# Performance work log

Measured on AMD Instinct MI355X. Metric: run time of the kernel, lower is better.

The kernel has to match this reference:

```python
import jax, jax.numpy as jnp
import numpy as np
from jax import lax

C = 128      # channels
H = 128
W = 128
B = 2
WS = 4       # window size
HEADS = 4
HID = int(C * 2.66)  # 340
EPS = 1e-6


def conv1x1(x, w):
    # x: [b,c,h,w], w: [out,in]
    return jnp.einsum('oc,bchw->bohw', w, x)


def dwconv3(x, w):
    # depthwise 3x3, w: [c,1,3,3]
    return lax.conv_general_dilated(
        x, w, window_strides=(1, 1), padding='SAME',
        feature_group_count=x.shape[1],
        dimension_numbers=('NCHW', 'OIHW', 'NCHW'))


def layernorm(x, w, b):
    # channel-wise LN over dim 1 (per pixel), w/b: [C]
    m = x.mean(axis=1, keepdims=True)
    v = ((x - m) ** 2).mean(axis=1, keepdims=True)
    xn = (x - m) / jnp.sqrt(v + EPS)
    return xn * w[None, :, None, None] + b[None, :, None, None]


def l2norm(x):
    n = jnp.sqrt(jnp.sum(x * x, axis=-1, keepdims=True))
    return x / jnp.maximum(n, 1e-12)


def rsa(x, qkv_w, dw_w, proj_w, temp):
    b, c, h, w = x.shape
    ws = WS
    x_ = jnp.roll(x, (-ws // 2, -ws // 2), axis=(2, 3))  # shifts > 0
    qkv = dwconv3(conv1x1(x_, qkv_w), dw_w)
    q, k, v = jnp.split(qkv, 3, axis=1)

    def win(t):  # b c (h dh) (w dw) -> b (h w) (dh dw) c
        return t.reshape(b, c, h // ws, ws, w // ws, ws) \
                .transpose(0, 2, 4, 3, 5, 1) \
                .reshape(b, (h // ws) * (w // ws), ws * ws, c)

    q, k, v = win(q), win(k), win(v)
    q = l2norm(q)
    k = l2norm(k)
    # attn = q^T @ k  -> [b, nw, c, c]
    attn = jax.nn.relu(jnp.einsum('bnpc,bnpd->bncd', q, k) * temp[0, 0, 0])
    out = jnp.einsum('bnpc,bncd->bnpd', v, attn)  # v @ attn
    out = out.reshape(b, h // ws, w // ws, ws, ws, c) \
             .transpose(0, 5, 1, 3, 2, 4).reshape(b, c, h, w)
    out = jnp.roll(out, (ws // 2, ws // 2), axis=(2, 3))
    return conv1x1(out, proj_w)


def gsa(x, qkv_w, dw_w, proj_w, temp):
    b, c, h, w = x.shape
    hd = HEADS
    ch = c // hd
    qkv = dwconv3(conv1x1(x, qkv_w), dw_w)
    q, k, v = jnp.split(qkv, 3, axis=1)

    def hs(t):  # b (head c) h w -> b head c (h w)
        return t.reshape(b, hd, ch, h * w)

    q, k, v = hs(q), hs(k), hs(v)
    q = l2norm(q)
    k = l2norm(k)
    attn = jax.nn.relu(jnp.einsum('bhcn,bhdn->bhcd', q, k) * temp[0, 0, 0])
    out = jnp.einsum('bhcd,bhdn->bhcn', attn, v).reshape(b, c, h, w)
    return conv1x1(out, proj_w)


def ffn(x, w_in, w_dw, w_out):
    h = dwconv3(conv1x1(x, w_in), w_dw)
    h = jax.nn.gelu(h, approximate=False)
    return conv1x1(h, w_out)


def setup_inputs() -> dict:
    key = jax.random.key(0)
    ks = jax.random.split(key, 16)
    s = 0.05
    d = {
        'x': jax.random.normal(ks[0], (B, C, H, W), jnp.float32),
        # spatial (RSA) branch
        'w_s0': jnp.ones((C,), jnp.float32), 'b_s0': jnp.zeros((C,), jnp.float32),
        'w_s2': jnp.ones((C,), jnp.float32), 'b_s2': jnp.zeros((C,), jnp.float32),
        'rsa_qkv': jax.random.normal(ks[1], (3 * C, C), jnp.float32) * s,
        'rsa_dw': jax.random.normal(ks[2], (3 * C, 1, 3, 3), jnp.float32) * s,
        'rsa_proj': jax.random.normal(ks[3], (C, C), jnp.float32) * s,
        'rsa_temp': jnp.ones((1, 1, 1), jnp.float32),
        'ffs_in': jax.random.normal(ks[4], (HID, C), jnp.float32) * s,
        'ffs_dw': jax.random.normal(ks[5], (HID, 1, 3, 3), jnp.float32) * s,
        'ffs_out': jax.random.normal(ks[6], (C, HID), jnp.float32) * s,
        # channel (GSA) branch
        'w_c0': jnp.ones((C,), jnp.float32), 'b_c0': jnp.zeros((C,), jnp.float32),
        'w_c2': jnp.ones((C,), jnp.float32), 'b_c2': jnp.zeros((C,), jnp.float32),
        'gsa_qkv': jax.random.normal(ks[7], (3 * C, C), jnp.float32) * s,
        'gsa_dw': jax.random.normal(ks[8], (3 * C, 1, 3, 3), jnp.float32) * s,
        'gsa_proj': jax.random.normal(ks[9], (C, C), jnp.float32) * s,
        'gsa_temp': jnp.ones((1, 1, 1), jnp.float32),
        'ffc_in': jax.random.normal(ks[10], (HID, C), jnp.float32) * s,
        'ffc_dw': jax.random.normal(ks[11], (HID, 1, 3, 3), jnp.float32) * s,
        'ffc_out': jax.random.normal(ks[12], (C, HID), jnp.float32) * s,
    }
    return d


def reference(x, w_s0, b_s0, w_s2, b_s2, rsa_qkv, rsa_dw, rsa_proj, rsa_temp,
              ffs_in, ffs_dw, ffs_out,
              w_c0, b_c0, w_c2, b_c2, gsa_qkv, gsa_dw, gsa_proj, gsa_temp,
              ffc_in, ffc_dw, ffc_out):
    # shared_depth = 1: only the i==0 branches execute
    # spatial block (RSA)
    x_ = rsa(layernorm(x, w_s0, b_s0), rsa_qkv, rsa_dw, rsa_proj, rsa_temp)
    x = ffn(layernorm(x_ + x, w_s2, b_s2), ffs_in, ffs_dw, ffs_out) + x_
    # channel block (GSA)
    x_ = gsa(layernorm(x, w_c0, b_c0), gsa_qkv, gsa_dw, gsa_proj, gsa_temp)
    x = ffn(layernorm(x_ + x, w_c2, b_c2), ffc_in, ffc_dw, ffc_out) + x_
    return x
```

## Files before the change

### kernel.cpp

```cpp
#include <hip/hip_runtime.h>
#include <hip/hip_bf16.h>
#include <math.h>

typedef __hip_bfloat16 bf16;
typedef __attribute__((ext_vector_type(8))) short short8;
typedef __attribute__((ext_vector_type(4))) short short4v;
typedef __attribute__((ext_vector_type(4))) float float4v;

static constexpr int cB  = 2;
static constexpr int cC  = 128;
static constexpr int cH  = 128;
static constexpr int cW  = 128;
static constexpr int cP  = cH * cW;
static constexpr int cC3 = 384;
static constexpr int cHID = 340;
static constexpr int cNW = 1024;
static constexpr float cEPS = 1e-6f;

__device__ __forceinline__ float bfu2f(unsigned short u){
  union { unsigned int i; float f; } c; c.i = ((unsigned int)u) << 16; return c.f;
}
__device__ __forceinline__ unsigned short f2b(float f){
  union { float f; unsigned int u; } c; c.f = f;
  unsigned int r = c.u + 0x7FFFu + ((c.u >> 16) & 1u);
  return (unsigned short)(r >> 16);
}

__global__ void k_wcvt(const float* __restrict__ qkv_s, const float* __restrict__ qkv_c,
                       const float* __restrict__ fin_s, const float* __restrict__ fin_c,
                       const float* __restrict__ prj_s, const float* __restrict__ prj_c,
                       const float* __restrict__ fo_s,  const float* __restrict__ fo_c,
                       unsigned short* __restrict__ WB, float* __restrict__ S){
  int i = blockIdx.x * 256 + threadIdx.x;
  if (i >= 319488){
    int j = i - 319488;
    if (j < 8704) S[j] = 0.f;
    return;
  }
  float v;
  if (i < 98304){
    v = (i < 49152) ? qkv_s[i] : qkv_c[i - 49152];
  } else if (i < 196608){
    int j = (i < 147456) ? (i - 98304) : (i - 147456);
    int row = j >> 7, col = j & 127;
    const float* src = (i < 147456) ? fin_s : fin_c;
    v = (row < cHID) ? src[row * 128 + col] : 0.f;
  } else if (i < 229376){
    v = (i < 212992) ? prj_s[i - 196608] : prj_c[i - 212992];
  } else {
    int j = (i < 274432) ? (i - 229376) : (i - 274432);
    int row = j / 352, col = j - row * 352;
    const float* src = (i < 274432) ? fo_s : fo_c;
    v = (col < cHID) ? src[row * cHID + col] : 0.f;
  }
  WB[i] = f2b(v);
}

__global__ void __launch_bounds__(256) k_gemmLN(const unsigned short* __restrict__ Wb,
                                                const float* __restrict__ Xf,
                                                const float* __restrict__ gamma,
                                                const float* __restrict__ beta,
                                                unsigned short* __restrict__ Out){
  __shared__ short Xls[64 * 136];
  __shared__ short Wls[128 * 40];
  __shared__ float gls[128], bls[128];
  __shared__ float psum[64], pssq[64];
  int bid = blockIdx.x;
  int s  = (bid & 7) * 192 + (bid >> 3);
  int mt = s % 3;
  int r3 = s / 3;
  int pt = r3 & 255;
  int b  = r3 >> 8;
  int p0 = pt * 64;
  int m0 = mt * 128;
  int t  = threadIdx.x;
  int px = t & 63, cq = t >> 6;
  if (t < 64){ psum[t] = 0.f; pssq[t] = 0.f; }
  if (t < 128){ gls[t] = gamma[t]; bls[t] = beta[t]; }
  int rh = p0 >> 7, w0 = p0 & 127;
  int hs = (rh + 2) & (cH - 1);
  int sp = hs * cW + ((w0 + 2 + px) & (cW - 1));
  const float* xb = Xf + (size_t)b * cC * cP + sp;
  float xr[32];
  float s1 = 0.f, s2 = 0.f;
  #pragma unroll
  for (int j = 0; j < 32; j++){
    float v = xb[(size_t)(cq * 32 + j) * cP];
    xr[j] = v; s1 += v; s2 += v * v;
  }
  __syncthreads();
  atomicAdd(&psum[px], s1);
  atomicAdd(&pssq[px], s2);
  __syncthreads();
  float mean = psum[px] * (1.f / cC);
  float var  = pssq[px] * (1.f / cC) - mean * mean;
  float rstd = rsqrtf(var + cEPS);
  #pragma unroll
  for (int k = 0; k < 4; k++){
    short8 tv;
    #pragma unroll
    for (int e = 0; e < 8; e++){
      int c = cq * 32 + k * 8 + e;
      tv[e] = (short)f2b((xr[k * 8 + e] - mean) * rstd * gls[c] + bls[c]);
    }
    *(short8*)&Xls[px * 136 + cq * 32 + k * 8] = tv;
  }
  int lanelo = t & 15;
  int quad   = (t >> 4) & 3;
  int wv = t >> 6;
  int w1 = wv & 1;
  int w2 = wv >> 1;
  int srw = t >> 1;
  int kow = (t & 1) * 16;
  float4v acc[2][4];
  #pragma unroll
  for (int i = 0; i < 2; i++)
    #pragma unroll
    for (int j = 0; j < 4; j++)
      acc[i][j] = (float4v){0.f, 0.f, 0.f, 0.f};
  const unsigned short* Wp = Wb + (size_t)(m0 + srw) * 128 + kow;
  short8 a0 = *(const short8*)(Wp);
  short8 a1 = *(const short8*)(Wp + 8);
  for (int k0 = 0; k0 < 128; k0 += 32){
    __syncthreads();
    *(short8*)&Wls[srw * 40 + kow]     = a0;
    *(short8*)&Wls[srw * 40 + kow + 8] = a1;
    __syncthreads();
    if (k0 < 96){
      a0 = *(const short8*)(Wp + k0 + 32);
      a1 = *(const short8*)(Wp + k0 + 40);
    }
    short8 af[2], bfr[4];
    #pragma unroll
    for (int i = 0; i < 2; i++)
      af[i] = *(const short8*)&Xls[(w1 * 32 + i * 16 + lanelo) * 136 + k0 + quad * 8];
    #pragma unroll
    for (int j = 0; j < 4; j++)
      bfr[j] = *(const short8*)&Wls[(w2 * 64 + j * 16 + lanelo) * 40 + quad * 8];
    #pragma unroll
    for (int i = 0; i < 2; i++)
      #pragma unroll
      for (int j = 0; j < 4; j++)
        acc[i][j] = __builtin_amdgcn_mfma_f32_16x16x32_bf16(af[i], bfr[j], acc[i][j], 0, 0, 0);
  }
  __syncthreads();
  #pragma unroll
  for (int i = 0; i < 2; i++)
    #pragma unroll
    for (int j = 0; j < 4; j++){
      int pixloc = w1 * 32 + i * 16 + quad * 4;
      int mloc   = w2 * 64 + j * 16 + lanelo;
      #pragma unroll
      for (int r = 0; r < 4; r++)
        Xls[(pixloc + r) * 136 + mloc] = (short)f2b(acc[i][j][r]);
    }
  __syncthreads();
  unsigned short* Ob = Out + (size_t)b * cP * cC3;
  #pragma unroll
  for (int rr = 0; rr < 4; rr++){
    int id = t + rr * 256;
    int row = id >> 4, col8 = (id & 15) * 8;
    *(short8*)(Ob + (size_t)(p0 + row) * cC3 + m0 + col8) = *(const short8*)&Xls[row * 136 + col8];
  }
}

__global__ void __launch_bounds__(256) k_gemm(const unsigned short* __restrict__ Wb,
                                              const unsigned short* __restrict__ Xg,
                                              unsigned short* __restrict__ Out,
                                              int K, int PK, int PM){
  __shared__ short SMEM[8704];
  short* Wls = SMEM;
  short* Xls = SMEM + 5120;
  int bid = blockIdx.x;
  int s  = (bid & 7) * (1536 >> 3) + (bid >> 3);
  int mt = s % 3;
  int r3 = s / 3;
  int pt = r3 & 255;
  int b  = r3 >> 8;
  int p0 = pt * 64;
  int m0 = mt * 128;
  int t  = threadIdx.x;
  int lanelo = t & 15;
  int quad   = (t >> 4) & 3;
  int wv = t >> 6;
  int w1 = wv & 1;
  int w2 = wv >> 1;
  int srw = t >> 1;
  int kow = (t & 1) * 16;
  int srx = t >> 2;
  int kox = (t & 3) * 8;

  float4v acc[2][4];
  #pragma unroll
  for (int i = 0; i < 2; i++)
    #pragma unroll
    for (int j = 0; j < 4; j++)
      acc[i][j] = (float4v){0.f, 0.f, 0.f, 0.f};

  const unsigned short* Xp = Xg + (size_t)b * cP * PK + (size_t)(p0 + srx) * PK + kox;
  const unsigned short* Wp = Wb + (size_t)(m0 + srw) * K + kow;

  short8 xv  = *(const short8*)(Xp);
  short8 wv0 = *(const short8*)(Wp);
  short8 wv1 = *(const short8*)(Wp + 8);
  for (int k0 = 0; k0 < K; k0 += 32){
    __syncthreads();
    *(short8*)&Wls[srw * 40 + kow]     = wv0;
    *(short8*)&Wls[srw * 40 + kow + 8] = wv1;
    *(short8*)&Xls[srx * 40 + kox]     = xv;
    __syncthreads();
    if (k0 + 32 < K){
      xv  = *(const short8*)(Xp + k0 + 32);
      wv0 = *(const short8*)(Wp + k0 + 32);
      wv1 = *(const short8*)(Wp + k0 + 40);
    }
    short8 af[2], bfr[4];
    #pragma unroll
    for (int i = 0; i < 2; i++)
      af[i] = *(const short8*)&Xls[(w1 * 32 + i * 16 + lanelo) * 40 + quad * 8];
    #pragma unroll
    for (int j = 0; j < 4; j++)
      bfr[j] = *(const short8*)&Wls[(w2 * 64 + j * 16 + lanelo) * 40 + quad * 8];
    #pragma unroll
    for (int i = 0; i < 2; i++)
      #pragma unroll
      for (int j = 0; j < 4; j++)
        acc[i][j] = __builtin_amdgcn_mfma_f32_16x16x32_bf16(af[i], bfr[j], acc[i][j], 0, 0, 0);
  }
  __syncthreads();
  #pragma unroll
  for (int i = 0; i < 2; i++)
    #pragma unroll
    for (int j = 0; j < 4; j++){
      int pixloc = w1 * 32 + i * 16 + quad * 4;
      int mloc   = w2 * 64 + j * 16 + lanelo;
      #pragma unroll
      for (int r = 0; r < 4; r++)
        SMEM[(pixloc + r) * 136 + mloc] = (short)f2b(acc[i][j][r]);
    }
  __syncthreads();
  unsigned short* Ob = Out + (size_t)b * cP * PM;
  #pragma unroll
  for (int rr = 0; rr < 4; rr++){
    int id = t + rr * 256;
    int row = id >> 4, col8 = (id & 15) * 8;
    int wcol = m0 + col8;
    if (wcol < PM)
      *(short8*)(Ob + (size_t)(p0 + row) * PM + wcol) = *(const short8*)&SMEM[row * 136 + col8];
  }
}

template<int MODE>
__global__ void __launch_bounds__(256) k_gemm64(const unsigned short* __restrict__ Wb,
                                                const unsigned short* __restrict__ Xg,
                                                const float* __restrict__ R,
                                                const float* __restrict__ Base,
                                                const float* __restrict__ gamma,
                                                const float* __restrict__ beta,
                                                float* __restrict__ Tr,
                                                unsigned short* __restrict__ LNo,
                                                int K, int PK){
  __shared__ short SMEM[8704];
  __shared__ float gls[128], bls[128];
  __shared__ float psum[64], pssq[64];
  short* Wls = SMEM;
  short* Xls = SMEM + 5120;
  int b  = blockIdx.z;
  int p0 = blockIdx.x * 64;
  int t  = threadIdx.x;
  int lanelo = t & 15;
  int quad   = (t >> 4) & 3;
  int wv = t >> 6;
  int w2 = wv >> 1, w1 = wv & 1;
  int srw = t >> 1;
  int kow = (t & 1) * 16;
  int srx = t >> 2;
  int kox = (t & 3) * 8;

  if (MODE != 3){
    if (t < 128){ gls[t] = gamma[t]; bls[t] = beta[t]; }
    if (t < 64){ psum[t] = 0.f; pssq[t] = 0.f; }
  }

  float4v acc[4][2];
  #pragma unroll
  for (int i = 0; i < 4; i++){
    acc[i][0] = (float4v){0.f, 0.f, 0.f, 0.f};
    acc[i][1] = (float4v){0.f, 0.f, 0.f, 0.f};
  }
  const unsigned short* Xp = Xg + (size_t)b * cP * PK + (size_t)(p0 + srx) * PK + kox;
  const unsigned short* Wp = Wb + (size_t)srw * K + kow;

  short8 xv  = *(const short8*)(Xp);
  short8 wv0 = *(const short8*)(Wp);
  short8 wv1 = *(const short8*)(Wp + 8);
  for (int k0 = 0; k0 < K; k0 += 32){
    __syncthreads();
    *(short8*)&Wls[srw * 40 + kow]     = wv0;
    *(short8*)&Wls[srw * 40 + kow + 8] = wv1;
    *(short8*)&Xls[srx * 40 + kox]     = xv;
    __syncthreads();
    if (k0 + 32 < K){
      xv  = *(const short8*)(Xp + k0 + 32);
      wv0 = *(const short8*)(Wp + k0 + 32);
      wv1 = *(const short8*)(Wp + k0 + 40);
    }
    short8 af[4], bfr[2];
    #pragma unroll
    for (int i = 0; i < 4; i++)
      af[i] = *(const short8*)&Wls[(w2 * 64 + i * 16 + lanelo) * 40 + quad * 8];
    #pragma unroll
    for (int j = 0; j < 2; j++)
      bfr[j] = *(const short8*)&Xls[(w1 * 32 + j * 16 + lanelo) * 40 + quad * 8];
    #pragma unroll
    for (int i = 0; i < 4; i++)
      #pragma unroll
      for (int j = 0; j < 2; j++)
        acc[i][j] = __builtin_amdgcn_mfma_f32_16x16x32_bf16(af[i], bfr[j], acc[i][j], 0, 0, 0);
  }
  float lnv[4][2][4];
  #pragma unroll
  for (int i = 0; i < 4; i++)
    #pragma unroll
    for (int j = 0; j < 2; j++){
      int n = p0 + w1 * 32 + j * 16 + lanelo;
      #pragma unroll
      for (int r = 0; r < 4; r++){
        int m = w2 * 64 + i * 16 + quad * 4 + r;
        size_t idx = (size_t)b * cC * cP + (size_t)m * cP + n;
        float v = acc[i][j][r];
        if (MODE >= 2) v += R[idx];
        Tr[idx] = v;
        if (MODE == 1) v += Base[idx];
        lnv[i][j][r] = v;
      }
    }
  if (MODE == 3) return;
  __syncthreads();
  #pragma unroll
  for (int j = 0; j < 2; j++){
    int nl = w1 * 32 + j * 16 + lanelo;
    float s = 0.f, ss = 0.f;
    #pragma unroll
    for (int i = 0; i < 4; i++)
      #pragma unroll
      for (int r = 0; r < 4; r++){
        float v = lnv[i][j][r];
        s += v; ss += v * v;
      }
    atomicAdd(&psum[nl], s);
    atomicAdd(&pssq[nl], ss);
  }
  __syncthreads();
  #pragma unroll
  for (int j = 0; j < 2; j++){
    int nl = w1 * 32 + j * 16 + lanelo;
    float mean = psum[nl] * (1.f / cC);
    float var = pssq[nl] * (1.f / cC) - mean * mean;
    float rstd = rsqrtf(var + cEPS);
    #pragma unroll
    for (int i = 0; i < 4; i++)
      #pragma unroll
      for (int r = 0; r < 4; r++){
        int m = w2 * 64 + i * 16 + quad * 4 + r;
        SMEM[nl * 136 + m] = (short)f2b((lnv[i][j][r] - mean) * rstd * gls[m] + bls[m]);
      }
  }
  __syncthreads();
  unsigned short* Ob = LNo + (size_t)b * cP * cC;
  #pragma unroll
  for (int rr = 0; rr < 4; rr++){
    int id = t + rr * 256;
    int row = id >> 4, col8 = (id & 15) * 8;
    short8 sv = *(const short8*)&SMEM[row * 136 + col8];
    *(short8*)(Ob + (size_t)(p0 + row) * cC + col8) = sv;
  }
}

template<int GELU, int CCn, int PITCH>
__global__ void __launch_bounds__(256) k_dw(const unsigned short* __restrict__ in,
                                            const float* __restrict__ wt,
                                            unsigned short* __restrict__ out){
  __shared__ float wls[16 * 76];
  int t = threadIdx.x;
  int cbase = blockIdx.y * 128;
  for (int i = t; i < 16 * 72; i += 256){
    int cg = i / 72, rem = i - cg * 72;
    int tap = rem >> 3, j = rem & 7;
    int c = cbase + cg * 8 + j;
    wls[cg * 76 + rem] = (c < CCn) ? wt[c * 9 + tap] : 0.f;
  }
  __syncthreads();
  int cgl = t & 15, pixl = t >> 4;
  int c0 = cbase + cgl * 8;
  if (c0 >= PITCH) return;
  int p = blockIdx.x * 16 + pixl;
  int h = p >> 7, w = p & 127;
  int b = blockIdx.z;
  const unsigned short* ib = in + (size_t)b * cP * PITCH;
  float4 wreg[18];
  #pragma unroll
  for (int q = 0; q < 18; q++)
    wreg[q] = *(const float4*)&wls[cgl * 76 + q * 4];
  short8 v[9];
  #pragma unroll
  for (int ky = 0; ky < 3; ky++){
    int hh = h + ky - 1;
    bool okh = (unsigned)hh < (unsigned)cH;
    int hc = okh ? hh : h;
    #pragma unroll
    for (int kx = 0; kx < 3; kx++){
      int ww = w + kx - 1;
      bool okw = (unsigned)ww < (unsigned)cW;
      int wc = okw ? ww : w;
      short8 lv = *(const short8*)(ib + (size_t)(hc * cW + wc) * PITCH + c0);
      if (!(okh && okw)) lv = (short8){0,0,0,0,0,0,0,0};
      v[ky * 3 + kx] = lv;
    }
  }
  float acc[8] = {0,0,0,0,0,0,0,0};
  #pragma unroll
  for (int tap = 0; tap < 9; tap++){
    float4 w0 = wreg[tap * 2];
    float4 w1 = wreg[tap * 2 + 1];
    float wa[8] = {w0.x, w0.y, w0.z, w0.w, w1.x, w1.y, w1.z, w1.w};
    #pragma unroll
    for (int j = 0; j < 8; j++)
      acc[j] += wa[j] * bfu2f((unsigned short)v[tap][j]);
  }
  short8 ov;
  #pragma unroll
  for (int j = 0; j < 8; j++){
    float vv = acc[j];
    if (GELU) vv = 0.5f * vv * (1.f + erff(vv * 0.70710678118654752f));
    ov[j] = (short)f2b(vv);
  }
  *(short8*)(out + (size_t)b * cP * PITCH + (size_t)p * PITCH + c0) = ov;
}

__global__ void __launch_bounds__(256) k_rsadw(const unsigned short* __restrict__ qkv,
                                               const float* __restrict__ wt,
                                               const float* __restrict__ temp,
                                               unsigned short* __restrict__ out){
  constexpr int QT = 0;
  constexpr int KT = 5120;
  constexpr int VO = 10240;
  constexpr int HA = 12416;
  constexpr int AT = 12416;
  __shared__ short lds[26528];
  __shared__ float nq[16], nk[16];
  int blk = blockIdx.x;
  int b  = blk >> 10;
  int nw = blk & 1023;
  int hb = nw >> 5, wb = nw & 31;
  int t = threadIdx.x;
  #pragma unroll
  for (int j = 0; j < 5; j++)
    *(short8*)&lds[t * 40 + j * 8] = (short8){0,0,0,0,0,0,0,0};
  if (t < 16) nq[t] = 0.f;
  else if (t < 32) nk[t - 16] = 0.f;
  __syncthreads();
  const unsigned short* base = qkv + (size_t)b * cP * cC3;
  #pragma unroll
  for (int r = 0; r < 7; r++){
    int i = t + 256 * r;
    if (i < 1728){
      int pix6 = i / 48;
      int cg = i - pix6 * 48;
      int hy = pix6 / 6, wx = pix6 - hy * 6;
      int hh = hb * 4 + hy - 1;
      int ww = wb * 4 + wx - 1;
      short8 v = (short8){0,0,0,0,0,0,0,0};
      if ((unsigned)hh < (unsigned)cH && (unsigned)ww < (unsigned)cW)
        v = *(const short8*)(base + (size_t)(hh * cW + ww) * cC3 + cg * 8);
      *(short8*)&lds[HA + pix6 * 392 + cg * 8] = v;
    }
  }
  __syncthreads();
  {
    int px = t & 15, grp = t >> 4;
    int py = px >> 2, pw = px & 3;
    #pragma unroll
    for (int g = 0; g < 3; g++){
      int c0 = grp * 24 + g * 8;
      const float4* wq = (const float4*)(wt + (size_t)c0 * 9);
      float wa[72];
      #pragma unroll
      for (int q = 0; q < 18; q++){
        float4 v4 = wq[q];
        wa[q * 4 + 0] = v4.x; wa[q * 4 + 1] = v4.y;
        wa[q * 4 + 2] = v4.z; wa[q * 4 + 3] = v4.w;
      }
      float acc8[8] = {0,0,0,0,0,0,0,0};
      #pragma unroll
      for (int ky = 0; ky < 3; ky++)
        #pragma unroll
        for (int kx = 0; kx < 3; kx++){
          short8 iv = *(const short8*)&lds[HA + ((py + ky) * 6 + pw + kx) * 392 + c0];
          int tap = ky * 3 + kx;
          #pragma unroll
          for (int e = 0; e < 8; e++)
            acc8[e] += wa[e * 9 + tap] * bfu2f((unsigned short)iv[e]);
        }
      if (c0 < 256){
        int isQ = c0 < 128;
        int off = isQ ? (QT + c0 * 40) : (KT + (c0 - 128) * 40);
        float s = 0.f;
        #pragma unroll
        for (int e = 0; e < 8; e++){
          unsigned short us = f2b(acc8[e]);
          float f = bfu2f(us);
          s += f * f;
          lds[off + e * 40 + px] = (short)us;
        }
        atomicAdd(isQ ? &nq[px] : &nk[px], s);
      } else {
        short8 sv;
        #pragma unroll
        for (int e = 0; e < 8; e++) sv[e] = (short)f2b(acc8[e]);
        *(short8*)&lds[VO + px * 136 + (c0 - 256)] = sv;
      }
    }
  }
  __syncthreads();
  float T = temp[0];
  #pragma unroll
  for (int r = 0; r < 8; r++){
    int idx = t + 256 * r;
    int c = idx >> 4, p = idx & 15;
    float sc = (1.f / fmaxf(sqrtf(nq[p]), 1e-12f)) * (1.f / fmaxf(sqrtf(nk[p]), 1e-12f));
    int a = QT + c * 40 + p;
    lds[a] = (short)f2b(bfu2f((unsigned short)lds[a]) * sc);
  }
  __syncthreads();
  int lanelo = t & 15;
  int quad = (t >> 4) & 3;
  int wv = t >> 6;
  float4v oacc[2];
  oacc[0] = (float4v){0.f,0.f,0.f,0.f};
  oacc[1] = (float4v){0.f,0.f,0.f,0.f};
  for (int ch = 0; ch < 2; ch++){
    #pragma unroll
    for (int ct = 0; ct < 4; ct++){
      int c0 = ch * 64 + ct * 16;
      short8 af = *(const short8*)&lds[QT + (c0 + lanelo) * 40 + quad * 8];
      #pragma unroll
      for (int dt = 0; dt < 2; dt++){
        int d0 = wv * 32 + dt * 16;
        short8 bf = *(const short8*)&lds[KT + (d0 + lanelo) * 40 + quad * 8];
        float4v acc = __builtin_amdgcn_mfma_f32_16x16x32_bf16(af, bf,
                        (float4v){0.f,0.f,0.f,0.f}, 0, 0, 0);
        short4v sv;
        #pragma unroll
        for (int r2 = 0; r2 < 4; r2++) sv[r2] = (short)f2b(fmaxf(acc[r2] * T, 0.f));
        *(short4v*)&lds[AT + (d0 + lanelo) * 72 + ct * 16 + quad * 4] = sv;
      }
    }
    __syncthreads();
    #pragma unroll
    for (int dt = 0; dt < 2; dt++){
      int d0 = wv * 32 + dt * 16;
      #pragma unroll
      for (int kk = 0; kk < 2; kk++){
        short8 av8 = *(const short8*)&lds[VO + lanelo * 136 + ch * 64 + kk * 32 + quad * 8];
        short8 bv8 = *(const short8*)&lds[AT + (d0 + lanelo) * 72 + kk * 32 + quad * 8];
        oacc[dt] = __builtin_amdgcn_mfma_f32_16x16x32_bf16(av8, bv8, oacc[dt], 0, 0, 0);
      }
    }
    __syncthreads();
  }
  #pragma unroll
  for (int dt = 0; dt < 2; dt++){
    int d = wv * 32 + dt * 16 + lanelo;
    #pragma unroll
    for (int r2 = 0; r2 < 4; r2++){
      int p = quad * 4 + r2;
      lds[p * 136 + d] = (short)f2b(oacc[dt][r2]);
    }
  }
  __syncthreads();
  {
    int px = t >> 4, cg = (t & 15) * 8;
    int h2 = (hb * 4 + (px >> 2) + 2) & (cH - 1);
    int w2 = (wb * 4 + (px & 3) + 2) & (cW - 1);
    short8 sv = *(const short8*)&lds[px * 136 + cg];
    *(short8*)(out + (size_t)b * cP * cC + (size_t)(h2 * cW + w2) * cC + cg) = sv;
  }
}

__global__ void __launch_bounds__(256) k_gram(const unsigned short* __restrict__ qkv,
                                              float* __restrict__ S,
                                              float* __restrict__ Qn,
                                              float* __restrict__ Kn){
  __shared__ float qs[32][132];
  __shared__ float ks[32][132];
  int blk = blockIdx.x;
  int chunk = blk & 127;
  int bh = blk >> 7;
  int b = bh >> 2, hd = bh & 3;
  int n0 = chunk * 128;
  int t = threadIdx.x;
  {
    int row = t >> 1;
    int half = t & 1;
    const unsigned short* pq = qkv + (size_t)b * cP * cC3 + (size_t)(n0 + row) * cC3 + hd * 32 + half * 16;
    const unsigned short* pk = pq + 128;
    short8 q0 = *(const short8*)pq;
    short8 q1 = *(const short8*)(pq + 8);
    short8 k0 = *(const short8*)pk;
    short8 k1 = *(const short8*)(pk + 8);
    #pragma unroll
    for (int e = 0; e < 8; e++){
      qs[half * 16 + e][row]     = bfu2f((unsigned short)q0[e]);
      qs[half * 16 + 8 + e][row] = bfu2f((unsigned short)q1[e]);
      ks[half * 16 + e][row]     = bfu2f((unsigned short)k0[e]);
      ks[half * 16 + 8 + e][row] = bfu2f((unsigned short)k1[e]);
    }
  }
  __syncthreads();
  if (t < 64){
    const float* row = (t < 32) ? qs[t] : ks[t - 32];
    float s = 0.f;
    #pragma unroll
    for (int i = 0; i < 128; i += 4){
      float4 v = *(const float4*)(row + i);
      s += v.x*v.x + v.y*v.y + v.z*v.z + v.w*v.w;
    }
    if (t < 32) atomicAdd(&Qn[bh * 32 + t], s);
    else        atomicAdd(&Kn[bh * 32 + (t - 32)], s);
  }
  int cc = (t >> 4) * 2;
  int dd = t & 15;
  float a00 = 0.f, a01 = 0.f, a10 = 0.f, a11 = 0.f;
  for (int n = 0; n < 128; n += 4){
    float4 q0 = *(const float4*)&qs[cc][n];
    float4 q1 = *(const float4*)&qs[cc + 1][n];
    float4 k0 = *(const float4*)&ks[dd][n];
    float4 k1 = *(const float4*)&ks[dd + 16][n];
    a00 += q0.x*k0.x + q0.y*k0.y + q0.z*k0.z + q0.w*k0.w;
    a01 += q0.x*k1.x + q0.y*k1.y + q0.z*k1.z + q0.w*k1.w;
    a10 += q1.x*k0.x + q1.y*k0.y + q1.z*k0.z + q1.w*k0.w;
    a11 += q1.x*k1.x + q1.y*k1.y + q1.z*k1.z + q1.w*k1.w;
  }
  float* Sb = S + (size_t)bh * 1024;
  atomicAdd(&Sb[cc * 32 + dd], a00);
  atomicAdd(&Sb[cc * 32 + dd + 16], a01);
  atomicAdd(&Sb[(cc + 1) * 32 + dd], a10);
  atomicAdd(&Sb[(cc + 1) * 32 + dd + 16], a11);
}

__global__ void __launch_bounds__(256) k_applyM(const unsigned short* __restrict__ qkv,
                                                const float* __restrict__ S,
                                                const float* __restrict__ Qn,
                                                const float* __restrict__ Kn,
                                                const float* __restrict__ temp,
                                                unsigned short* __restrict__ out){
  __shared__ short atb[128 * 40];
  __shared__ short OT[64 * 136];
  int b = blockIdx.y;
  int nbase = blockIdx.x * 64;
  int t = threadIdx.x;
  float T = temp[0];
  #pragma unroll
  for (int it = 0; it < 16; it++){
    int i = t + it * 256;
    int c = i >> 5, d = i & 31;
    int hd = c >> 5, cl = c & 31;
    int bh = b * 4 + hd;
    float nqv = fmaxf(sqrtf(Qn[bh * 32 + cl]), 1e-12f);
    float nkv = fmaxf(sqrtf(Kn[bh * 32 + d]), 1e-12f);
    float v = fmaxf(S[(size_t)bh * 1024 + cl * 32 + d] / (nqv * nkv) * T, 0.f);
    atb[c * 40 + d] = (short)f2b(v);
  }
  __syncthreads();
  int lanelo = t & 15, quad = (t >> 4) & 3, wv = t >> 6;
  int n0 = nbase + wv * 16;
  const unsigned short* vb = qkv + (size_t)b * cP * cC3 + (size_t)(n0 + lanelo) * cC3 + 256 + quad * 8;
  #pragma unroll
  for (int hd = 0; hd < 4; hd++){
    short8 af = *(const short8*)(vb + hd * 32);
    #pragma unroll
    for (int cth = 0; cth < 2; cth++){
      int c0 = hd * 32 + cth * 16;
      short8 bf = *(const short8*)&atb[(c0 + lanelo) * 40 + quad * 8];
      float4v acc = __builtin_amdgcn_mfma_f32_16x16x32_bf16(af, bf,
                      (float4v){0.f,0.f,0.f,0.f}, 0, 0, 0);
      #pragma unroll
      for (int r = 0; r < 4; r++)
        OT[(wv * 16 + quad * 4 + r) * 136 + c0 + lanelo] = (short)f2b(acc[r]);
    }
  }
  __syncthreads();
  unsigned short* ob = out + (size_t)b * cP * cC;
  #pragma unroll
  for (int rr = 0; rr < 4; rr++){
    int id = t + rr * 256;
    int row = id >> 4, col8 = (id & 15) * 8;
    *(short8*)(ob + (size_t)(nbase + row) * cC + col8) = *(const short8*)&OT[row * 136 + col8];
  }
}

extern "C" void kernel_launch(void* const* d_in, const int* in_sizes, int n_in,
                              void* d_out, int out_size, void* d_ws, size_t ws_size,
                              hipStream_t stream){
  const float* x     = (const float*)d_in[0];
  const float* w_s0  = (const float*)d_in[1];
  const float* b_s0  = (const float*)d_in[2];
  const float* w_s2  = (const float*)d_in[3];
  const float* b_s2  = (const float*)d_in[4];
  const float* rsa_qkv  = (const float*)d_in[5];
  const float* rsa_dw   = (const float*)d_in[6];
  const float* rsa_proj = (const float*)d_in[7];
  const float* rsa_temp = (const float*)d_in[8];
  const float* ffs_in   = (const float*)d_in[9];
  const float* ffs_dw   = (const float*)d_in[10];
  const float* ffs_out  = (const float*)d_in[11];
  const float* w_c0  = (const float*)d_in[12];
  const float* b_c0  = (const float*)d_in[13];
  const float* w_c2  = (const float*)d_in[14];
  const float* b_c2  = (const float*)d_in[15];
  const float* gsa_qkv  = (const float*)d_in[16];
  const float* gsa_dw   = (const float*)d_in[17];
  const float* gsa_proj = (const float*)d_in[18];
  const float* gsa_temp = (const float*)d_in[19];
  const float* ffc_in   = (const float*)d_in[20];
  const float* ffc_dw   = (const float*)d_in[21];
  const float* ffc_out  = (const float*)d_in[22];

  const size_t szC  = (size_t)cB * cC * cP;
  const size_t szC3 = (size_t)cB * cC3 * cP;
  float* XF = (float*)d_ws;
  float* XS = XF + szC;
  unsigned short* LO   = (unsigned short*)(XS + szC);
  unsigned short* Abuf = LO + szC;
  unsigned short* Bbuf = Abuf + szC3;
  float* S  = (float*)(Bbuf + szC3);
  float* Qn = S + 8192;
  float* Kn = Qn + 256;
  float* AT = Kn + 256;
  unsigned short* WB = (unsigned short*)(AT + 1024);
  unsigned short* W_QKV_S = WB;
  unsigned short* W_QKV_C = WB + 49152;
  unsigned short* W_FIN_S = WB + 98304;
  unsigned short* W_FIN_C = WB + 147456;
  unsigned short* W_PRJ_S = WB + 196608;
  unsigned short* W_PRJ_C = WB + 212992;
  unsigned short* W_FO_S  = WB + 229376;
  unsigned short* W_FO_C  = WB + 274432;

  dim3 t256(256);
  dim3 gG1(cP / 64 * 3 * cB);
  dim3 gG64(cP / 64, 1, cB);
  dim3 gDW(cP / 16, 3, cB);

  k_wcvt<<<dim3(1282), t256, 0, stream>>>(rsa_qkv, gsa_qkv, ffs_in, ffc_in,
                                          rsa_proj, gsa_proj, ffs_out, ffc_out, WB, S);

  k_gemmLN<<<gG1, t256, 0, stream>>>(W_QKV_S, x, w_s0, b_s0, Abuf);
  k_rsadw<<<dim3(cB * cNW), t256, 0, stream>>>(Abuf, rsa_dw, rsa_temp, LO);
  k_gemm64<1><<<gG64, t256, 0, stream>>>(W_PRJ_S, LO, nullptr, x, w_s2, b_s2, XS, LO, 128, 128);
  k_gemm<<<gG1, t256, 0, stream>>>(W_FIN_S, LO, Abuf, 128, 128, 352);
  k_dw<1,340,352><<<gDW, t256, 0, stream>>>(Abuf, ffs_dw, Bbuf);
  k_gemm64<2><<<gG64, t256, 0, stream>>>(W_FO_S, Bbuf, XS, nullptr, w_c0, b_c0, XF, LO, 352, 352);

  k_gemm<<<gG1, t256, 0, stream>>>(W_QKV_C, LO, Abuf, 128, 128, 384);
  k_dw<0,384,384><<<gDW, t256, 0, stream>>>(Abuf, gsa_dw, Bbuf);
  k_gram<<<dim3(1024), t256, 0, stream>>>(Bbuf, S, Qn, Kn);
  k_applyM<<<dim3(cP / 64, cB), t256, 0, stream>>>(Bbuf, S, Qn, Kn, gsa_temp, LO);
  k_gemm64<1><<<gG64, t256, 0, stream>>>(W_PRJ_C, LO, nullptr, XF, w_c2, b_c2, XS, LO, 128, 128);
  k_gemm<<<gG1, t256, 0, stream>>>(W_FIN_C, LO, Abuf, 128, 128, 352);
  k_dw<1,340,352><<<gDW, t256, 0, stream>>>(Abuf, ffc_dw, Bbuf);
  k_gemm64<3><<<gG64, t256, 0, stream>>>(W_FO_C, Bbuf, XS, nullptr, nullptr, nullptr,
                                         (float*)d_out, nullptr, 352, 352);
}
```

Before: 332.9 us.

## Fuse depthwise 3x3 convs into consuming GEMM, gram and apply kernels

Removes the standalone depthwise-conv kernels. The 3x3 depthwise conv (plus GELU for the FFN paths) is computed on the fly inside the FFN output GEMM's B-operand staging and inside the GSA gram and apply kernels. This drops the write and re-read of the intermediate Bbuf tensor and three launches per block. In exchange it recomputes the depthwise conv in both the gram and apply kernels for V/Q/K, adds nine gathered loads per K-step in the GEMM, and raises LDS use for the depthwise weights.

```diff
diff --git a/kernel.cpp b/kernel.cpp
--- a/kernel.cpp
+++ b/kernel.cpp
@@ -377,65 +377,164 @@
   }
 }
 
-template<int GELU, int CCn, int PITCH>
-__global__ void __launch_bounds__(256) k_dw(const unsigned short* __restrict__ in,
-                                            const float* __restrict__ wt,
-                                            unsigned short* __restrict__ out){
-  __shared__ float wls[16 * 76];
-  int t = threadIdx.x;
-  int cbase = blockIdx.y * 128;
-  for (int i = t; i < 16 * 72; i += 256){
-    int cg = i / 72, rem = i - cg * 72;
-    int tap = rem >> 3, j = rem & 7;
-    int c = cbase + cg * 8 + j;
-    wls[cg * 76 + rem] = (c < CCn) ? wt[c * 9 + tap] : 0.f;
-  }
-  __syncthreads();
-  int cgl = t & 15, pixl = t >> 4;
-  int c0 = cbase + cgl * 8;
-  if (c0 >= PITCH) return;
-  int p = blockIdx.x * 16 + pixl;
-  int h = p >> 7, w = p & 127;
-  int b = blockIdx.z;
-  const unsigned short* ib = in + (size_t)b * cP * PITCH;
-  float4 wreg[18];
-  #pragma unroll
-  for (int q = 0; q < 18; q++)
-    wreg[q] = *(const float4*)&wls[cgl * 76 + q * 4];
-  short8 v[9];
+template<int MODE>
+__global__ void __launch_bounds__(256) k_gemm64dw(const unsigned short* __restrict__ Wb,
+                                                  const unsigned short* __restrict__ Ain,
+                                                  const float* __restrict__ dww,
+                                                  const float* __restrict__ R,
+                                                  const float* __restrict__ gamma,
+                                                  const float* __restrict__ beta,
+                                                  float* __restrict__ Tr,
+                                                  unsigned short* __restrict__ LNo){
+  constexpr int K = 352, PK = 352;
+  __shared__ short SMEM[8704];
+  __shared__ float gls[128], bls[128];
+  __shared__ float psum[64], pssq[64];
+  __shared__ float wdw[352 * 9];
+  short* Wls = SMEM;
+  short* Xls = SMEM + 5120;
+  int b  = blockIdx.z;
+  int p0 = blockIdx.x * 64;
+  int t  = threadIdx.x;
+  for (int i = t; i < 3168; i += 256){
+    int c = i / 9;
+    wdw[i] = (c < cHID) ? dww[i] : 0.f;
+  }
+  if (MODE == 2){
+    if (t < 128){ gls[t] = gamma[t]; bls[t] = beta[t]; }
+    if (t < 64){ psum[t] = 0.f; pssq[t] = 0.f; }
+  }
+  int lanelo = t & 15;
+  int quad   = (t >> 4) & 3;
+  int wv = t >> 6;
+  int w2 = wv >> 1, w1 = wv & 1;
+  int srw = t >> 1;
+  int kow = (t & 1) * 16;
+  int srx = t >> 2;
+  int kox = (t & 3) * 8;
+  int pix = p0 + srx, h = pix >> 7, w = pix & 127;
+  const unsigned short* Ab = Ain + (size_t)b * cP * PK;
+  const unsigned short* rb[3];
+  bool okh[3], okw[3];
   #pragma unroll
   for (int ky = 0; ky < 3; ky++){
-    int hh = h + ky - 1;
-    bool okh = (unsigned)hh < (unsigned)cH;
-    int hc = okh ? hh : h;
-    #pragma unroll
-    for (int kx = 0; kx < 3; kx++){
-      int ww = w + kx - 1;
-      bool okw = (unsigned)ww < (unsigned)cW;
-      int wc = okw ? ww : w;
-      short8 lv = *(const short8*)(ib + (size_t)(hc * cW + wc) * PITCH + c0);
-      if (!(okh && okw)) lv = (short8){0,0,0,0,0,0,0,0};
-      v[ky * 3 + kx] = lv;
-    }
-  }
-  float acc[8] = {0,0,0,0,0,0,0,0};
-  #pragma unroll
-  for (int tap = 0; tap < 9; tap++){
-    float4 w0 = wreg[tap * 2];
-    float4 w1 = wreg[tap * 2 + 1];
-    float wa[8] = {w0.x, w0.y, w0.z, w0.w, w1.x, w1.y, w1.z, w1.w};
-    #pragma unroll
-    for (int j = 0; j < 8; j++)
-      acc[j] += wa[j] * bfu2f((unsigned short)v[tap][j]);
-  }
-  short8 ov;
-  #pragma unroll
-  for (int j = 0; j < 8; j++){
-    float vv = acc[j];
-    if (GELU) vv = 0.5f * vv * (1.f + erff(vv * 0.70710678118654752f));
-    ov[j] = (short)f2b(vv);
-  }
-  *(short8*)(out + (size_t)b * cP * PITCH + (size_t)p * PITCH + c0) = ov;
+    okh[ky] = (unsigned)(h + ky - 1) < (unsigned)cH;
+    rb[ky] = Ab + ((size_t)(h + ky - 1) * cW + (w - 1)) * PK + kox;
+  }
+  okw[0] = (w > 0); okw[1] = true; okw[2] = (w < cW - 1);
+
+  float4v acc[4][2];
+  #pragma unroll
+  for (int i = 0; i < 4; i++){
+    acc[i][0] = (float4v){0.f, 0.f, 0.f, 0.f};
+    acc[i][1] = (float4v){0.f, 0.f, 0.f, 0.f};
+  }
+  const unsigned short* Wp = Wb + (size_t)srw * K + kow;
+  short8 wv0 = *(const short8*)(Wp);
+  short8 wv1 = *(const short8*)(Wp + 8);
+  short8 tp[9];
+  #pragma unroll
+  for (int ky = 0; ky < 3; ky++)
+    #pragma unroll
+    for (int kx = 0; kx < 3; kx++)
+      tp[ky * 3 + kx] = (okh[ky] && okw[kx]) ? *(const short8*)(rb[ky] + kx * PK)
+                                             : (short8){0,0,0,0,0,0,0,0};
+  __syncthreads();
+  for (int k0 = 0; k0 < K; k0 += 32){
+    short8 xv;
+    #pragma unroll
+    for (int e = 0; e < 8; e++){
+      int c = k0 + kox + e;
+      float a = 0.f;
+      #pragma unroll
+      for (int q = 0; q < 9; q++)
+        a += wdw[c * 9 + q] * bfu2f((unsigned short)tp[q][e]);
+      a = 0.5f * a * (1.f + erff(a * 0.70710678118654752f));
+      xv[e] = (short)f2b(a);
+    }
+    __syncthreads();
+    *(short8*)&Wls[srw * 40 + kow]     = wv0;
+    *(short8*)&Wls[srw * 40 + kow + 8] = wv1;
+    *(short8*)&Xls[srx * 40 + kox]     = xv;
+    __syncthreads();
+    if (k0 + 32 < K){
+      wv0 = *(const short8*)(Wp + k0 + 32);
+      wv1 = *(const short8*)(Wp + k0 + 40);
+      #pragma unroll
+      for (int ky = 0; ky < 3; ky++)
+        #pragma unroll
+        for (int kx = 0; kx < 3; kx++)
+          tp[ky * 3 + kx] = (okh[ky] && okw[kx]) ? *(const short8*)(rb[ky] + kx * PK + k0 + 32)
+                                                 : (short8){0,0,0,0,0,0,0,0};
+    }
+    short8 af[4], bfr[2];
+    #pragma unroll
+    for (int i = 0; i < 4; i++)
+      af[i] = *(const short8*)&Wls[(w2 * 64 + i * 16 + lanelo) * 40 + quad * 8];
+    #pragma unroll
+    for (int j = 0; j < 2; j++)
+      bfr[j] = *(const short8*)&Xls[(w1 * 32 + j * 16 + lanelo) * 40 + quad * 8];
+    #pragma unroll
+    for (int i = 0; i < 4; i++)
+      #pragma unroll
+      for (int j = 0; j < 2; j++)
+        acc[i][j] = __builtin_amdgcn_mfma_f32_16x16x32_bf16(af[i], bfr[j], acc[i][j], 0, 0, 0);
+  }
+  float lnv[4][2][4];
+  #pragma unroll
+  for (int i = 0; i < 4; i++)
+    #pragma unroll
+    for (int j = 0; j < 2; j++){
+      int n = p0 + w1 * 32 + j * 16 + lanelo;
+      #pragma unroll
+      for (int r = 0; r < 4; r++){
+        int m = w2 * 64 + i * 16 + quad * 4 + r;
+        size_t idx = (size_t)b * cC * cP + (size_t)m * cP + n;
+        float v = acc[i][j][r] + R[idx];
+        Tr[idx] = v;
+        lnv[i][j][r] = v;
+      }
+    }
+  if (MODE == 3) return;
+  __syncthreads();
+  #pragma unroll
+  for (int j = 0; j < 2; j++){
+    int nl = w1 * 32 + j * 16 + lanelo;
+    float s = 0.f, ss = 0.f;
+    #pragma unroll
+    for (int i = 0; i < 4; i++)
+      #pragma unroll
+      for (int r = 0; r < 4; r++){
+        float v = lnv[i][j][r];
+        s += v; ss += v * v;
+      }
+    atomicAdd(&psum[nl], s);
+    atomicAdd(&pssq[nl], ss);
+  }
+  __syncthreads();
+  #pragma unroll
+  for (int j = 0; j < 2; j++){
+    int nl = w1 * 32 + j * 16 + lanelo;
+    float mean = psum[nl] * (1.f / cC);
+    float var = pssq[nl] * (1.f / cC) - mean * mean;
+    float rstd = rsqrtf(var + cEPS);
+    #pragma unroll
+    for (int i = 0; i < 4; i++)
+      #pragma unroll
+      for (int r = 0; r < 4; r++){
+        int m = w2 * 64 + i * 16 + quad * 4 + r;
+        SMEM[nl * 136 + m] = (short)f2b((lnv[i][j][r] - mean) * rstd * gls[m] + bls[m]);
+      }
+  }
+  __syncthreads();
+  unsigned short* Ob = LNo + (size_t)b * cP * cC;
+  #pragma unroll
+  for (int rr = 0; rr < 4; rr++){
+    int id = t + rr * 256;
+    int row = id >> 4, col8 = (id & 15) * 8;
+    short8 sv = *(const short8*)&SMEM[row * 136 + col8];
+    *(short8*)(Ob + (size_t)(p0 + row) * cC + col8) = sv;
+  }
 }
 
 __global__ void __launch_bounds__(256) k_rsadw(const unsigned short* __restrict__ qkv,
@@ -588,42 +687,67 @@
   }
 }
 
-__global__ void __launch_bounds__(256) k_gram(const unsigned short* __restrict__ qkv,
-                                              float* __restrict__ S,
-                                              float* __restrict__ Qn,
-                                              float* __restrict__ Kn){
+__global__ void __launch_bounds__(256) k_gramdw(const unsigned short* __restrict__ Ain,
+                                                const float* __restrict__ dww,
+                                                float* __restrict__ S,
+                                                float* __restrict__ Qn,
+                                                float* __restrict__ Kn){
   __shared__ float qs[32][132];
   __shared__ float ks[32][132];
+  __shared__ float wdw[576];
   int blk = blockIdx.x;
   int chunk = blk & 127;
   int bh = blk >> 7;
   int b = bh >> 2, hd = bh & 3;
-  int n0 = chunk * 128;
   int t = threadIdx.x;
-  {
-    int row = t >> 1;
-    int half = t & 1;
-    const unsigned short* pq = qkv + (size_t)b * cP * cC3 + (size_t)(n0 + row) * cC3 + hd * 32 + half * 16;
-    const unsigned short* pk = pq + 128;
-    short8 q0 = *(const short8*)pq;
-    short8 q1 = *(const short8*)(pq + 8);
-    short8 k0 = *(const short8*)pk;
-    short8 k1 = *(const short8*)(pk + 8);
-    #pragma unroll
-    for (int e = 0; e < 8; e++){
-      qs[half * 16 + e][row]     = bfu2f((unsigned short)q0[e]);
-      qs[half * 16 + 8 + e][row] = bfu2f((unsigned short)q1[e]);
-      ks[half * 16 + e][row]     = bfu2f((unsigned short)k0[e]);
-      ks[half * 16 + 8 + e][row] = bfu2f((unsigned short)k1[e]);
-    }
+  for (int i = t; i < 576; i += 256){
+    int lc = i / 9, tpq = i - lc * 9;
+    int c = (lc < 32) ? (hd * 32 + lc) : (128 + hd * 32 + (lc - 32));
+    wdw[i] = dww[c * 9 + tpq];
+  }
+  __syncthreads();
+  int row = t >> 1;
+  int half = t & 1;
+  int h = chunk, w = row;
+  const unsigned short* Ab = Ain + (size_t)b * cP * cC3;
+  float qa[16], ka[16];
+  #pragma unroll
+  for (int e = 0; e < 16; e++){ qa[e] = 0.f; ka[e] = 0.f; }
+  #pragma unroll
+  for (int ky = 0; ky < 3; ky++){
+    int hh = h + ky - 1;
+    if ((unsigned)hh >= (unsigned)cH) continue;
+    #pragma unroll
+    for (int kx = 0; kx < 3; kx++){
+      int ww = w + kx - 1;
+      if ((unsigned)ww >= (unsigned)cW) continue;
+      const unsigned short* pp = Ab + (size_t)(hh * cW + ww) * cC3 + hd * 32 + half * 16;
+      short8 q0 = *(const short8*)pp;
+      short8 q1 = *(const short8*)(pp + 8);
+      short8 k0v = *(const short8*)(pp + 128);
+      short8 k1v = *(const short8*)(pp + 136);
+      int tpi = ky * 3 + kx;
+      #pragma unroll
+      for (int e = 0; e < 8; e++){
+        qa[e]     += wdw[(half * 16 + e) * 9 + tpi]          * bfu2f((unsigned short)q0[e]);
+        qa[8 + e] += wdw[(half * 16 + 8 + e) * 9 + tpi]      * bfu2f((unsigned short)q1[e]);
+        ka[e]     += wdw[(32 + half * 16 + e) * 9 + tpi]     * bfu2f((unsigned short)k0v[e]);
+        ka[8 + e] += wdw[(32 + half * 16 + 8 + e) * 9 + tpi] * bfu2f((unsigned short)k1v[e]);
+      }
+    }
+  }
+  #pragma unroll
+  for (int e = 0; e < 16; e++){
+    qs[half * 16 + e][row] = bfu2f(f2b(qa[e]));
+    ks[half * 16 + e][row] = bfu2f(f2b(ka[e]));
   }
   __syncthreads();
   if (t < 64){
-    const float* row = (t < 32) ? qs[t] : ks[t - 32];
+    const float* rowp = (t < 32) ? qs[t] : ks[t - 32];
     float s = 0.f;
     #pragma unroll
     for (int i = 0; i < 128; i += 4){
-      float4 v = *(const float4*)(row + i);
+      float4 v = *(const float4*)(rowp + i);
       s += v.x*v.x + v.y*v.y + v.z*v.z + v.w*v.w;
     }
     if (t < 32) atomicAdd(&Qn[bh * 32 + t], s);
@@ -649,18 +773,22 @@
   atomicAdd(&Sb[(cc + 1) * 32 + dd + 16], a11);
 }
 
-__global__ void __launch_bounds__(256) k_applyM(const unsigned short* __restrict__ qkv,
-                                                const float* __restrict__ S,
-                                                const float* __restrict__ Qn,
-                                                const float* __restrict__ Kn,
-                                                const float* __restrict__ temp,
-                                                unsigned short* __restrict__ out){
+__global__ void __launch_bounds__(256) k_applydw(const unsigned short* __restrict__ Ain,
+                                                 const float* __restrict__ dww,
+                                                 const float* __restrict__ S,
+                                                 const float* __restrict__ Qn,
+                                                 const float* __restrict__ Kn,
+                                                 const float* __restrict__ temp,
+                                                 unsigned short* __restrict__ out){
   __shared__ short atb[128 * 40];
   __shared__ short OT[64 * 136];
+  __shared__ float wdw[1152];
   int b = blockIdx.y;
   int nbase = blockIdx.x * 64;
   int t = threadIdx.x;
   float T = temp[0];
+  for (int i = t; i < 1152; i += 256)
+    wdw[i] = dww[2304 + i];
   #pragma unroll
   for (int it = 0; it < 16; it++){
     int i = t + it * 256;
@@ -674,11 +802,30 @@
   }
   __syncthreads();
   int lanelo = t & 15, quad = (t >> 4) & 3, wv = t >> 6;
-  int n0 = nbase + wv * 16;
-  const unsigned short* vb = qkv + (size_t)b * cP * cC3 + (size_t)(n0 + lanelo) * cC3 + 256 + quad * 8;
+  int pix = nbase + wv * 16 + lanelo;
+  int h = pix >> 7, w = pix & 127;
+  const unsigned short* Ab = Ain + (size_t)b * cP * cC3;
   #pragma unroll
   for (int hd = 0; hd < 4; hd++){
-    short8 af = *(const short8*)(vb + hd * 32);
+    float va[8] = {0,0,0,0,0,0,0,0};
+    #pragma unroll
+    for (int ky = 0; ky < 3; ky++){
+      int hh = h + ky - 1;
+      if ((unsigned)hh >= (unsigned)cH) continue;
+      #pragma unroll
+      for (int kx = 0; kx < 3; kx++){
+        int ww = w + kx - 1;
+        if ((unsigned)ww >= (unsigned)cW) continue;
+        short8 iv = *(const short8*)(Ab + (size_t)(hh * cW + ww) * cC3 + 256 + hd * 32 + quad * 8);
+        int tpi = ky * 3 + kx;
+        #pragma unroll
+        for (int e = 0; e < 8; e++)
+          va[e] += wdw[(hd * 32 + quad * 8 + e) * 9 + tpi] * bfu2f((unsigned short)iv[e]);
+      }
+    }
+    short8 af;
+    #pragma unroll
+    for (int e = 0; e < 8; e++) af[e] = (short)f2b(va[e]);
     #pragma unroll
     for (int cth = 0; cth < 2; cth++){
       int c0 = hd * 32 + cth * 16;
@@ -751,7 +898,6 @@
   dim3 t256(256);
   dim3 gG1(cP / 64 * 3 * cB);
   dim3 gG64(cP / 64, 1, cB);
-  dim3 gDW(cP / 16, 3, cB);
 
   k_wcvt<<<dim3(1282), t256, 0, stream>>>(rsa_qkv, gsa_qkv, ffs_in, ffc_in,
                                           rsa_proj, gsa_proj, ffs_out, ffc_out, WB, S);
@@ -760,16 +906,13 @@
   k_rsadw<<<dim3(cB * cNW), t256, 0, stream>>>(Abuf, rsa_dw, rsa_temp, LO);
   k_gemm64<1><<<gG64, t256, 0, stream>>>(W_PRJ_S, LO, nullptr, x, w_s2, b_s2, XS, LO, 128, 128);
   k_gemm<<<gG1, t256, 0, stream>>>(W_FIN_S, LO, Abuf, 128, 128, 352);
-  k_dw<1,340,352><<<gDW, t256, 0, stream>>>(Abuf, ffs_dw, Bbuf);
-  k_gemm64<2><<<gG64, t256, 0, stream>>>(W_FO_S, Bbuf, XS, nullptr, w_c0, b_c0, XF, LO, 352, 352);
+  k_gemm64dw<2><<<gG64, t256, 0, stream>>>(W_FO_S, Abuf, ffs_dw, XS, w_c0, b_c0, XF, LO);
 
   k_gemm<<<gG1, t256, 0, stream>>>(W_QKV_C, LO, Abuf, 128, 128, 384);
-  k_dw<0,384,384><<<gDW, t256, 0, stream>>>(Abuf, gsa_dw, Bbuf);
-  k_gram<<<dim3(1024), t256, 0, stream>>>(Bbuf, S, Qn, Kn);
-  k_applyM<<<dim3(cP / 64, cB), t256, 0, stream>>>(Bbuf, S, Qn, Kn, gsa_temp, LO);
+  k_gramdw<<<dim3(1024), t256, 0, stream>>>(Abuf, gsa_dw, S, Qn, Kn);
+  k_applydw<<<dim3(cP / 64, cB), t256, 0, stream>>>(Abuf, gsa_dw, S, Qn, Kn, gsa_temp, LO);
   k_gemm64<1><<<gG64, t256, 0, stream>>>(W_PRJ_C, LO, nullptr, XF, w_c2, b_c2, XS, LO, 128, 128);
   k_gemm<<<gG1, t256, 0, stream>>>(W_FIN_C, LO, Abuf, 128, 128, 352);
-  k_dw<1,340,352><<<gDW, t256, 0, stream>>>(Abuf, ffc_dw, Bbuf);
-  k_gemm64<3><<<gG64, t256, 0, stream>>>(W_FO_C, Bbuf, XS, nullptr, nullptr, nullptr,
-                                         (float*)d_out, nullptr, 352, 352);
-}
+  k_gemm64dw<3><<<gG64, t256, 0, stream>>>(W_FO_C, Abuf, ffc_dw, XS, nullptr, nullptr,
+                                           (float*)d_out, nullptr);
+}
```

New measurement: 355.8 us. 1.07x slower.

## Fuse GSA depthwise conv into gram and attention-apply kernels

Applied to the files above, without the earlier changes.

Removes the standalone depthwise 3x3 conv launch for the GSA qkv tensor. The gram kernel now computes the q/k depthwise conv on the fly from the pre-conv buffer, and the apply kernel computes the v conv inline, rounding to bf16 to match the previous intermediate. This drops a full write and re-read of the 384-channel intermediate. In exchange, each output pixel gathers nine neighbours directly from global memory with no shared-memory halo reuse, which adds redundant loads and ALU work.

```diff
diff --git a/kernel.cpp b/kernel.cpp
--- a/kernel.cpp
+++ b/kernel.cpp
@@ -588,42 +588,67 @@
   }
 }
 
-__global__ void __launch_bounds__(256) k_gram(const unsigned short* __restrict__ qkv,
-                                              float* __restrict__ S,
-                                              float* __restrict__ Qn,
-                                              float* __restrict__ Kn){
+__global__ void __launch_bounds__(256) k_gramdw(const unsigned short* __restrict__ Ain,
+                                                const float* __restrict__ dww,
+                                                float* __restrict__ S,
+                                                float* __restrict__ Qn,
+                                                float* __restrict__ Kn){
   __shared__ float qs[32][132];
   __shared__ float ks[32][132];
+  __shared__ float wdw[576];
   int blk = blockIdx.x;
   int chunk = blk & 127;
   int bh = blk >> 7;
   int b = bh >> 2, hd = bh & 3;
-  int n0 = chunk * 128;
   int t = threadIdx.x;
-  {
-    int row = t >> 1;
-    int half = t & 1;
-    const unsigned short* pq = qkv + (size_t)b * cP * cC3 + (size_t)(n0 + row) * cC3 + hd * 32 + half * 16;
-    const unsigned short* pk = pq + 128;
-    short8 q0 = *(const short8*)pq;
-    short8 q1 = *(const short8*)(pq + 8);
-    short8 k0 = *(const short8*)pk;
-    short8 k1 = *(const short8*)(pk + 8);
-    #pragma unroll
-    for (int e = 0; e < 8; e++){
-      qs[half * 16 + e][row]     = bfu2f((unsigned short)q0[e]);
-      qs[half * 16 + 8 + e][row] = bfu2f((unsigned short)q1[e]);
-      ks[half * 16 + e][row]     = bfu2f((unsigned short)k0[e]);
-      ks[half * 16 + 8 + e][row] = bfu2f((unsigned short)k1[e]);
-    }
+  for (int i = t; i < 576; i += 256){
+    int lc = i / 9, tpq = i - lc * 9;
+    int c = (lc < 32) ? (hd * 32 + lc) : (128 + hd * 32 + (lc - 32));
+    wdw[i] = dww[c * 9 + tpq];
+  }
+  __syncthreads();
+  int row = t >> 1;
+  int half = t & 1;
+  int h = chunk, w = row;
+  const unsigned short* Ab = Ain + (size_t)b * cP * cC3;
+  float qa[16], ka[16];
+  #pragma unroll
+  for (int e = 0; e < 16; e++){ qa[e] = 0.f; ka[e] = 0.f; }
+  #pragma unroll
+  for (int ky = 0; ky < 3; ky++){
+    int hh = h + ky - 1;
+    if ((unsigned)hh >= (unsigned)cH) continue;
+    #pragma unroll
+    for (int kx = 0; kx < 3; kx++){
+      int ww = w + kx - 1;
+      if ((unsigned)ww >= (unsigned)cW) continue;
+      const unsigned short* pp = Ab + (size_t)(hh * cW + ww) * cC3 + hd * 32 + half * 16;
+      short8 q0 = *(const short8*)pp;
+      short8 q1 = *(const short8*)(pp + 8);
+      short8 k0v = *(const short8*)(pp + 128);
+      short8 k1v = *(const short8*)(pp + 136);
+      int tpi = ky * 3 + kx;
+      #pragma unroll
+      for (int e = 0; e < 8; e++){
+        qa[e]     += wdw[(half * 16 + e) * 9 + tpi]          * bfu2f((unsigned short)q0[e]);
+        qa[8 + e] += wdw[(half * 16 + 8 + e) * 9 + tpi]      * bfu2f((unsigned short)q1[e]);
+        ka[e]     += wdw[(32 + half * 16 + e) * 9 + tpi]     * bfu2f((unsigned short)k0v[e]);
+        ka[8 + e] += wdw[(32 + half * 16 + 8 + e) * 9 + tpi] * bfu2f((unsigned short)k1v[e]);
+      }
+    }
+  }
+  #pragma unroll
+  for (int e = 0; e < 16; e++){
+    qs[half * 16 + e][row] = bfu2f(f2b(qa[e]));
+    ks[half * 16 + e][row] = bfu2f(f2b(ka[e]));
   }
   __syncthreads();
   if (t < 64){
-    const float* row = (t < 32) ? qs[t] : ks[t - 32];
+    const float* rowp = (t < 32) ? qs[t] : ks[t - 32];
     float s = 0.f;
     #pragma unroll
     for (int i = 0; i < 128; i += 4){
-      float4 v = *(const float4*)(row + i);
+      float4 v = *(const float4*)(rowp + i);
       s += v.x*v.x + v.y*v.y + v.z*v.z + v.w*v.w;
     }
     if (t < 32) atomicAdd(&Qn[bh * 32 + t], s);
@@ -649,18 +674,22 @@
   atomicAdd(&Sb[(cc + 1) * 32 + dd + 16], a11);
 }
 
-__global__ void __launch_bounds__(256) k_applyM(const unsigned short* __restrict__ qkv,
-                                                const float* __restrict__ S,
-                                                const float* __restrict__ Qn,
-                                                const float* __restrict__ Kn,
-                                                const float* __restrict__ temp,
-                                                unsigned short* __restrict__ out){
+__global__ void __launch_bounds__(256) k_applydw(const unsigned short* __restrict__ Ain,
+                                                 const float* __restrict__ dww,
+                                                 const float* __restrict__ S,
+                                                 const float* __restrict__ Qn,
+                                                 const float* __restrict__ Kn,
+                                                 const float* __restrict__ temp,
+                                                 unsigned short* __restrict__ out){
   __shared__ short atb[128 * 40];
   __shared__ short OT[64 * 136];
+  __shared__ float wdw[1152];
   int b = blockIdx.y;
   int nbase = blockIdx.x * 64;
   int t = threadIdx.x;
   float T = temp[0];
+  for (int i = t; i < 1152; i += 256)
+    wdw[i] = dww[2304 + i];
   #pragma unroll
   for (int it = 0; it < 16; it++){
     int i = t + it * 256;
@@ -674,11 +703,30 @@
   }
   __syncthreads();
   int lanelo = t & 15, quad = (t >> 4) & 3, wv = t >> 6;
-  int n0 = nbase + wv * 16;
-  const unsigned short* vb = qkv + (size_t)b * cP * cC3 + (size_t)(n0 + lanelo) * cC3 + 256 + quad * 8;
+  int pix = nbase + wv * 16 + lanelo;
+  int h = pix >> 7, w = pix & 127;
+  const unsigned short* Ab = Ain + (size_t)b * cP * cC3;
   #pragma unroll
   for (int hd = 0; hd < 4; hd++){
-    short8 af = *(const short8*)(vb + hd * 32);
+    float va[8] = {0,0,0,0,0,0,0,0};
+    #pragma unroll
+    for (int ky = 0; ky < 3; ky++){
+      int hh = h + ky - 1;
+      if ((unsigned)hh >= (unsigned)cH) continue;
+      #pragma unroll
+      for (int kx = 0; kx < 3; kx++){
+        int ww = w + kx - 1;
+        if ((unsigned)ww >= (unsigned)cW) continue;
+        short8 iv = *(const short8*)(Ab + (size_t)(hh * cW + ww) * cC3 + 256 + hd * 32 + quad * 8);
+        int tpi = ky * 3 + kx;
+        #pragma unroll
+        for (int e = 0; e < 8; e++)
+          va[e] += wdw[(hd * 32 + quad * 8 + e) * 9 + tpi] * bfu2f((unsigned short)iv[e]);
+      }
+    }
+    short8 af;
+    #pragma unroll
+    for (int e = 0; e < 8; e++) af[e] = (short)f2b(va[e]);
     #pragma unroll
     for (int cth = 0; cth < 2; cth++){
       int c0 = hd * 32 + cth * 16;
@@ -764,9 +812,8 @@
   k_gemm64<2><<<gG64, t256, 0, stream>>>(W_FO_S, Bbuf, XS, nullptr, w_c0, b_c0, XF, LO, 352, 352);
 
   k_gemm<<<gG1, t256, 0, stream>>>(W_QKV_C, LO, Abuf, 128, 128, 384);
-  k_dw<0,384,384><<<gDW, t256, 0, stream>>>(Abuf, gsa_dw, Bbuf);
-  k_gram<<<dim3(1024), t256, 0, stream>>>(Bbuf, S, Qn, Kn);
-  k_applyM<<<dim3(cP / 64, cB), t256, 0, stream>>>(Bbuf, S, Qn, Kn, gsa_temp, LO);
+  k_gramdw<<<dim3(1024), t256, 0, stream>>>(Abuf, gsa_dw, S, Qn, Kn);
+  k_applydw<<<dim3(cP / 64, cB), t256, 0, stream>>>(Abuf, gsa_dw, S, Qn, Kn, gsa_temp, LO);
   k_gemm64<1><<<gG64, t256, 0, stream>>>(W_PRJ_C, LO, nullptr, XF, w_c2, b_c2, XS, LO, 128, 128);
   k_gemm<<<gG1, t256, 0, stream>>>(W_FIN_C, LO, Abuf, 128, 128, 352);
   k_dw<1,340,352><<<gDW, t256, 0, stream>>>(Abuf, ffc_dw, Bbuf);
```

Result: no change. 334.2 us (+0.4%).
